# Optimization experiments

Hardware: AMD Instinct MI355X
Metric: run time of the kernel (lower is better)

## Reference

```python
import jax, jax.numpy as jnp
import numpy as np

EPS = 1e-08

def setup_inputs() -> dict:
    key = jax.random.key(0)
    k1, k2, k3, k4 = jax.random.split(key, 4)
    batch, n_in, n_out, D = 32768, 256, 512, 16
    x = jax.random.uniform(k1, (batch, n_in), jnp.float32, minval=-1.0, maxval=1.0)
    omega = jax.random.normal(k2, (D, 1), jnp.float32)          # stddev=1.0 init
    phase = 0.1 * jax.random.normal(k3, (D, 1), jnp.float32)    # zeros in module; small noise for non-degenerate test
    std_c = 1.0 / np.sqrt(n_in * D)
    c_basis = std_c * jax.random.normal(k4, (n_out, n_in, D), jnp.float32)
    bias = jnp.zeros((n_out,), jnp.float32)
    return {"x": x, "omega": omega, "phase": phase, "c_basis": c_basis, "bias": bias}

def _basis(x, omega, phase):
    # x: (batch, n_in) -> B: (batch, n_in, D)
    D = omega.shape[0]
    w = omega.reshape(1, 1, D)
    p = phase.reshape(1, 1, D)
    wx = w * x[..., None]
    s = jnp.sin(wx + p)
    mu = jnp.exp(-0.5 * w ** 2) * jnp.sin(p)
    std = jnp.sqrt(0.5 * (1.0 - jnp.exp(-2.0 * w ** 2) * jnp.cos(2.0 * p)) - mu ** 2)
    return (s + mu) / (std + EPS)

def reference(x, omega, phase, c_basis, bias):
    B = _basis(x, omega, phase)                     # (batch, n_in, D)
    y = jnp.einsum('bid,oid->bo', B, c_basis)       # (batch, n_out)
    return y + bias
```

## Files before the change

### kernel.cpp

```cpp
#include <hip/hip_runtime.h>
#include <hip/hip_bf16.h>


#define BATCH 32768
#define NIN   256
#define NOUT  512
#define DDIM  16
#define BM    128
#define BN    512
#define NKS   128
#define ASLICE 8192
#define BSLICE 32768
#define EPSV  1e-8f
#define INV2PI 0.15915494309189535f

typedef short  bf16x8 __attribute__((ext_vector_type(8)));
typedef float  f32x4  __attribute__((ext_vector_type(4)));

static __device__ __forceinline__ ushort f2bf(float f) {
  union { __hip_bfloat16 h; ushort u; } cv;
  cv.h = __float2bfloat16(f);
  return cv.u;
}

static __device__ __forceinline__ uint cvt_pk(float lo, float hi) {
  uint r;
  asm("v_cvt_pk_bf16_f32 %0, %1, %2" : "=v"(r) : "v"(lo), "v"(hi));
  return r;
}

__global__ __launch_bounds__(256) void prep_kernel(
    const float* __restrict__ omega, const float* __restrict__ phase,
    const float* __restrict__ c_basis, const float* __restrict__ bias,
    ushort* __restrict__ cb, float* __restrict__ offs)
{
  __shared__ float s_scale[DDIM];
  __shared__ float s_musc[DDIM];
  __shared__ float s_red[4];

  const int o = blockIdx.x;
  const int t = threadIdx.x;

  if (t < DDIM) {
    float w = omega[t];
    float p = phase[t];
    float mu  = expf(-0.5f * w * w) * sinf(p);
    float var = 0.5f * (1.0f - expf(-2.0f * w * w) * cosf(2.0f * p)) - mu * mu;
    float sd  = sqrtf(fmaxf(var, 0.0f));
    float sc  = 1.0f / (sd + EPSV);
    s_scale[t] = sc;
    s_musc[t]  = mu * sc;
  }
  __syncthreads();

  const float* cp = c_basis + ((size_t)o * NIN + t) * DDIM;
  float cv[DDIM];
  {
    const float4* cp4 = (const float4*)cp;
    float4 a = cp4[0], b = cp4[1], c = cp4[2], d = cp4[3];
    cv[0]=a.x; cv[1]=a.y; cv[2]=a.z; cv[3]=a.w;
    cv[4]=b.x; cv[5]=b.y; cv[6]=b.z; cv[7]=b.w;
    cv[8]=c.x; cv[9]=c.y; cv[10]=c.z; cv[11]=c.w;
    cv[12]=d.x; cv[13]=d.y; cv[14]=d.z; cv[15]=d.w;
  }

  float partial = 0.0f;
  uint pk[8];
#pragma unroll
  for (int d = 0; d < DDIM; d += 2) {
    partial += cv[d] * s_musc[d] + cv[d+1] * s_musc[d+1];
    ushort u0 = f2bf(cv[d]   * s_scale[d]);
    ushort u1 = f2bf(cv[d+1] * s_scale[d+1]);
    pk[d >> 1] = (uint)u0 | ((uint)u1 << 16);
  }

  {
    const int ks = t >> 1;
    const int h0 = (t & 1) * 2;
    const int fo = (o >> 1) & 3;
    char* rowp = (char*)cb + (size_t)ks * BSLICE + o * 64;
    *(uint4*)(rowp + ((h0    ) ^ fo) * 16) = make_uint4(pk[0], pk[1], pk[2], pk[3]);
    *(uint4*)(rowp + ((h0 + 1) ^ fo) * 16) = make_uint4(pk[4], pk[5], pk[6], pk[7]);
  }

#pragma unroll
  for (int off = 32; off > 0; off >>= 1) partial += __shfl_down(partial, off, 64);
  if ((t & 63) == 0) s_red[t >> 6] = partial;
  __syncthreads();
  if (t == 0) offs[o] = bias[o] + s_red[0] + s_red[1] + s_red[2] + s_red[3];
}

__global__ __launch_bounds__(512, 2) void gemm_kernel(
    const float* __restrict__ x, const float* __restrict__ omega,
    const float* __restrict__ phase, const ushort* __restrict__ cb,
    const float* __restrict__ offs, float* __restrict__ out)
{
  extern __shared__ char lds[];

  const int t    = threadIdx.x;
  const int lane = t & 63;
  const int wid  = t >> 6;
  const int wm   = wid >> 2;
  const int wn   = wid & 3;
  const int row0 = blockIdx.x * BM;

  f32x4 acc[4][8];
#pragma unroll
  for (int m = 0; m < 4; ++m)
#pragma unroll
    for (int n = 0; n < 8; ++n) acc[m][n] = (f32x4){0.f, 0.f, 0.f, 0.f};

  const int r   = t >> 2;
  const int sub = t & 3;
  const int il  = sub >> 1;
  const int d0  = (sub & 1) * 8;
  const float* xbase = x + (size_t)(row0 + r) * NIN + il;
  const int awa = r * 64 + ((sub ^ ((r >> 1) & 3)) * 16);

  float wvt[8], pvt[8];
#pragma unroll
  for (int j = 0; j < 8; ++j) {
    wvt[j] = omega[d0 + j] * INV2PI;
    pvt[j] = phase[d0 + j] * INV2PI;
  }

  const int hi  = lane >> 4;
  const int l15 = lane & 15;
  const int hu  = (hi ^ ((l15 >> 1) & 3)) * 16;

#define GLL(s_, d_) __builtin_amdgcn_global_load_lds(                          \
      (const __attribute__((address_space(1))) void*)(s_),                     \
      (__attribute__((address_space(3))) void*)(d_), 16, 0, 0)

#define ISSUE_B(ks_, slot_)                                                    \
  {                                                                            \
    const char* src = (const char*)cb + (size_t)(ks_) * BSLICE                 \
                      + wid * 1024 + lane * 16;                                \
    char* dst = lds + 32768 + (slot_) * BSLICE + wid * 1024;                   \
    GLL(src, dst);             GLL(src + 8192,  dst + 8192);                   \
    GLL(src + 16384, dst + 16384); GLL(src + 24576, dst + 24576);              \
  }

#define SINS4(xx_)                                                             \
    _Pragma("unroll")                                                          \
    for (int j = 0; j < 8; j += 2) {                                           \
      float s0 = __builtin_amdgcn_sinf(fmaf(wvt[j],     (xx_), pvt[j]));       \
      float s1 = __builtin_amdgcn_sinf(fmaf(wvt[j + 1], (xx_), pvt[j + 1]));   \
      pk[j >> 1] = cvt_pk(s0, s1);                                             \
    }

#define AWRITE(slot_)                                                          \
    *(uint4*)(lds + (slot_) * ASLICE + awa) = make_uint4(pk[0],pk[1],pk[2],pk[3]);

#define FRAG_MFMA(slot_)                                                       \
  {                                                                            \
    const char* AsB = lds + (slot_) * ASLICE;                                  \
    const char* BsB = lds + 32768 + (slot_) * BSLICE;                          \
    bf16x8 af[4];                                                              \
    _Pragma("unroll")                                                          \
    for (int m = 0; m < 4; ++m)                                                \
      af[m] = *(const bf16x8*)(AsB + (wm*64 + m*16 + l15) * 64 + hu);          \
    bf16x8 bfr[8];                                                             \
    _Pragma("unroll")                                                          \
    for (int n = 0; n < 8; ++n)                                                \
      bfr[n] = *(const bf16x8*)(BsB + (wn*128 + n*16 + l15) * 64 + hu);        \
    __builtin_amdgcn_s_setprio(1);                                             \
    _Pragma("unroll")                                                          \
    for (int m = 0; m < 4; ++m)                                                \
      _Pragma("unroll")                                                        \
      for (int n = 0; n < 8; ++n)                                              \
        acc[m][n] = __builtin_amdgcn_mfma_f32_16x16x32_bf16(af[m], bfr[n], acc[m][n], 0, 0, 0); \
    __builtin_amdgcn_s_setprio(0);                                             \
  }

#define BODY(s_, rd_, aw_, bg_, XU_, XL_)                                      \
  {                                                                            \
    ISSUE_B(((s_) + 3 < NKS ? (s_) + 3 : NKS - 1), bg_);                       \
    XL_ = xbase[((s_) + 3 < NKS ? (s_) + 3 : NKS - 1) * 2];                    \
    __builtin_amdgcn_sched_barrier(0);                                         \
    uint pk[4];                                                                \
    SINS4(XU_)                                                                 \
    AWRITE(aw_)                                                                \
    FRAG_MFMA(rd_)                                                             \
    __builtin_amdgcn_sched_barrier(0);                                         \
    asm volatile("s_waitcnt vmcnt(8) lgkmcnt(0)" ::: "memory");                \
    __builtin_amdgcn_s_barrier();                                              \
    __builtin_amdgcn_sched_barrier(0);                                         \
  }

  float xsA, xsB;
  {
    float xp0 = xbase[0];
    float xp1 = xbase[2];
    ISSUE_B(0, 0) ISSUE_B(1, 1) ISSUE_B(2, 2)
    xsA = xbase[4];
    uint pk[4];
    SINS4(xp0) AWRITE(0)
    SINS4(xp1) AWRITE(1)
    __builtin_amdgcn_sched_barrier(0);
    asm volatile("s_waitcnt vmcnt(0) lgkmcnt(0)" ::: "memory");
    __builtin_amdgcn_s_barrier();
    __builtin_amdgcn_sched_barrier(0);
  }

  for (int s = 0; s < NKS; s += 4) {
    BODY(s,     0, 2, 3, xsA, xsB)
    BODY(s + 1, 1, 3, 0, xsB, xsA)
    BODY(s + 2, 2, 0, 1, xsA, xsB)
    BODY(s + 3, 3, 1, 2, xsB, xsA)
  }

#pragma unroll
  for (int n = 0; n < 8; ++n) {
    int col = wn * 128 + n * 16 + l15;
    float off = offs[col];
#pragma unroll
    for (int m = 0; m < 4; ++m) {
      int row = row0 + wm * 64 + m * 16 + hi * 4;
      float* op = out + (size_t)row * NOUT + col;
#pragma unroll
      for (int j = 0; j < 4; ++j)
        op[(size_t)j * NOUT] = acc[m][n][j] + off;
    }
  }
}

extern "C" void kernel_launch(void* const* d_in, const int* in_sizes, int n_in,
                              void* d_out, int out_size, void* d_ws, size_t ws_size,
                              hipStream_t stream) {
  const float* x       = (const float*)d_in[0];
  const float* omega   = (const float*)d_in[1];
  const float* phase   = (const float*)d_in[2];
  const float* c_basis = (const float*)d_in[3];
  const float* bias    = (const float*)d_in[4];
  float* out = (float*)d_out;

  float*  offs = (float*)d_ws;
  ushort* cb   = (ushort*)((char*)d_ws + 2048);

  hipFuncSetAttribute((const void*)gemm_kernel,
                      hipFuncAttributeMaxDynamicSharedMemorySize, 163840);

  prep_kernel<<<NOUT, 256, 0, stream>>>(omega, phase, c_basis, bias, cb, offs);
  gemm_kernel<<<BATCH / BM, 512, 163840, stream>>>(x, omega, phase, cb, offs, out);
}
```

Baseline: 151.1 us.

## Compute A fragments in registers and give each wave private B slices without barriers

Each wave now computes its sin-basis A fragments straight into MFMA registers from x loads, instead of staging them through shared LDS. Each wave also double-buffers its own private slice of B, which removes all block-wide barriers. The block tile shrinks to 64 rows with 4 waves, and LDS use drops to 64KB. The cost is that every wave recomputes the same sines, four times redundant transcendental work per block, while B traffic per output row doubles because of the smaller BM and the prefetch depth drops from 3 to 1.

```diff
diff --git a/kernel.cpp b/kernel.cpp
--- a/kernel.cpp
+++ b/kernel.cpp
@@ -6,10 +6,9 @@
 #define NIN   256
 #define NOUT  512
 #define DDIM  16
-#define BM    128
+#define BM    64
 #define BN    512
 #define NKS   128
-#define ASLICE 8192
 #define BSLICE 32768
 #define EPSV  1e-8f
 #define INV2PI 0.15915494309189535f
@@ -90,7 +89,7 @@
   if (t == 0) offs[o] = bias[o] + s_red[0] + s_red[1] + s_red[2] + s_red[3];
 }
 
-__global__ __launch_bounds__(512, 2) void gemm_kernel(
+__global__ __launch_bounds__(256, 2) void gemm_kernel(
     const float* __restrict__ x, const float* __restrict__ omega,
     const float* __restrict__ phase, const ushort* __restrict__ cb,
     const float* __restrict__ offs, float* __restrict__ out)
@@ -99,35 +98,36 @@
 
   const int t    = threadIdx.x;
   const int lane = t & 63;
-  const int wid  = t >> 6;
-  const int wm   = wid >> 2;
-  const int wn   = wid & 3;
+  const int wn   = t >> 6;
   const int row0 = blockIdx.x * BM;
-
-  f32x4 acc[4][8];
-#pragma unroll
-  for (int m = 0; m < 4; ++m)
-#pragma unroll
-    for (int n = 0; n < 8; ++n) acc[m][n] = (f32x4){0.f, 0.f, 0.f, 0.f};
-
-  const int r   = t >> 2;
-  const int sub = t & 3;
-  const int il  = sub >> 1;
-  const int d0  = (sub & 1) * 8;
-  const float* xbase = x + (size_t)(row0 + r) * NIN + il;
-  const int awa = r * 64 + ((sub ^ ((r >> 1) & 3)) * 16);
-
-  float wvt[8], pvt[8];
-#pragma unroll
-  for (int j = 0; j < 8; ++j) {
-    wvt[j] = omega[d0 + j] * INV2PI;
-    pvt[j] = phase[d0 + j] * INV2PI;
-  }
 
   const int hi  = lane >> 4;
   const int l15 = lane & 15;
   const int hu  = (hi ^ ((l15 >> 1) & 3)) * 16;
 
+  float wl[8], pl[8];
+  {
+    const int dbase = (hi & 1) * 8;
+#pragma unroll
+    for (int j = 0; j < 8; ++j) {
+      wl[j] = omega[dbase + j] * INV2PI;
+      pl[j] = phase[dbase + j] * INV2PI;
+    }
+  }
+
+  const float* xp0 = x + (size_t)(row0 + 0 * 16 + l15) * NIN;
+  const float* xp1 = x + (size_t)(row0 + 1 * 16 + l15) * NIN;
+  const float* xp2 = x + (size_t)(row0 + 2 * 16 + l15) * NIN;
+  const float* xp3 = x + (size_t)(row0 + 3 * 16 + l15) * NIN;
+
+  f32x4 acc[4][8];
+#pragma unroll
+  for (int m = 0; m < 4; ++m)
+#pragma unroll
+    for (int n = 0; n < 8; ++n) acc[m][n] = (f32x4){0.f, 0.f, 0.f, 0.f};
+
+  char* ldsW = lds + wn * 16384;
+
 #define GLL(s_, d_) __builtin_amdgcn_global_load_lds(                          \
       (const __attribute__((address_space(1))) void*)(s_),                     \
       (__attribute__((address_space(3))) void*)(d_), 16, 0, 0)
@@ -135,35 +135,50 @@
 #define ISSUE_B(ks_, slot_)                                                    \
   {                                                                            \
     const char* src = (const char*)cb + (size_t)(ks_) * BSLICE                 \
-                      + wid * 1024 + lane * 16;                                \
-    char* dst = lds + 32768 + (slot_) * BSLICE + wid * 1024;                   \
-    GLL(src, dst);             GLL(src + 8192,  dst + 8192);                   \
-    GLL(src + 16384, dst + 16384); GLL(src + 24576, dst + 24576);              \
-  }
-
-#define SINS4(xx_)                                                             \
-    _Pragma("unroll")                                                          \
-    for (int j = 0; j < 8; j += 2) {                                           \
-      float s0 = __builtin_amdgcn_sinf(fmaf(wvt[j],     (xx_), pvt[j]));       \
-      float s1 = __builtin_amdgcn_sinf(fmaf(wvt[j + 1], (xx_), pvt[j + 1]));   \
-      pk[j >> 1] = cvt_pk(s0, s1);                                             \
-    }
-
-#define AWRITE(slot_)                                                          \
-    *(uint4*)(lds + (slot_) * ASLICE + awa) = make_uint4(pk[0],pk[1],pk[2],pk[3]);
-
-#define FRAG_MFMA(slot_)                                                       \
+                      + wn * 8192 + lane * 16;                                 \
+    char* dst = ldsW + (slot_) * 8192;                                         \
+    GLL(src, dst);               GLL(src + 1024, dst + 1024);                  \
+    GLL(src + 2048, dst + 2048); GLL(src + 3072, dst + 3072);                  \
+    GLL(src + 4096, dst + 4096); GLL(src + 5120, dst + 5120);                  \
+    GLL(src + 6144, dst + 6144); GLL(src + 7168, dst + 7168);                  \
+  }
+
+#define XLOAD(XV_, s_)                                                         \
+    XV_[0] = *(const float2*)(xp0 + 2 * (s_));                                 \
+    XV_[1] = *(const float2*)(xp1 + 2 * (s_));                                 \
+    XV_[2] = *(const float2*)(xp2 + 2 * (s_));                                 \
+    XV_[3] = *(const float2*)(xp3 + 2 * (s_));
+
+#define MAKE_AF(m_, XV_)                                                       \
   {                                                                            \
-    const char* AsB = lds + (slot_) * ASLICE;                                  \
-    const char* BsB = lds + 32768 + (slot_) * BSLICE;                          \
+    float xx = (hi & 2) ? XV_[m_].y : XV_[m_].x;                               \
+    uint w0 = cvt_pk(__builtin_amdgcn_sinf(fmaf(wl[0], xx, pl[0])),            \
+                     __builtin_amdgcn_sinf(fmaf(wl[1], xx, pl[1])));           \
+    uint w1 = cvt_pk(__builtin_amdgcn_sinf(fmaf(wl[2], xx, pl[2])),            \
+                     __builtin_amdgcn_sinf(fmaf(wl[3], xx, pl[3])));           \
+    uint w2 = cvt_pk(__builtin_amdgcn_sinf(fmaf(wl[4], xx, pl[4])),            \
+                     __builtin_amdgcn_sinf(fmaf(wl[5], xx, pl[5])));           \
+    uint w3 = cvt_pk(__builtin_amdgcn_sinf(fmaf(wl[6], xx, pl[6])),            \
+                     __builtin_amdgcn_sinf(fmaf(wl[7], xx, pl[7])));           \
+    uint2 lohi0 = make_uint2(w0, w1), lohi1 = make_uint2(w2, w3);              \
+    af[m_] = __builtin_bit_cast(bf16x8,                                        \
+              make_uint4(lohi0.x, lohi0.y, lohi1.x, lohi1.y));                 \
+  }
+
+#define BODY(s_, sl_, XU_, XL_)                                                \
+  {                                                                            \
+    const int ksn = ((s_) + 1 < NKS ? (s_) + 1 : NKS - 1);                     \
+    ISSUE_B(ksn, (sl_) ^ 1)                                                    \
+    XLOAD(XL_, ksn)                                                            \
+    __builtin_amdgcn_sched_barrier(0);                                         \
+    asm volatile("s_waitcnt vmcnt(16)" ::: "memory");                          \
     bf16x8 af[4];                                                              \
-    _Pragma("unroll")                                                          \
-    for (int m = 0; m < 4; ++m)                                                \
-      af[m] = *(const bf16x8*)(AsB + (wm*64 + m*16 + l15) * 64 + hu);          \
+    MAKE_AF(0, XU_) MAKE_AF(1, XU_) MAKE_AF(2, XU_) MAKE_AF(3, XU_)            \
+    const char* BsB = ldsW + (sl_) * 8192;                                     \
     bf16x8 bfr[8];                                                             \
     _Pragma("unroll")                                                          \
     for (int n = 0; n < 8; ++n)                                                \
-      bfr[n] = *(const bf16x8*)(BsB + (wn*128 + n*16 + l15) * 64 + hu);        \
+      bfr[n] = *(const bf16x8*)(BsB + (n * 16 + l15) * 64 + hu);               \
     __builtin_amdgcn_s_setprio(1);                                             \
     _Pragma("unroll")                                                          \
     for (int m = 0; m < 4; ++m)                                                \
@@ -173,41 +188,14 @@
     __builtin_amdgcn_s_setprio(0);                                             \
   }
 
-#define BODY(s_, rd_, aw_, bg_, XU_, XL_)                                      \
-  {                                                                            \
-    ISSUE_B(((s_) + 3 < NKS ? (s_) + 3 : NKS - 1), bg_);                       \
-    XL_ = xbase[((s_) + 3 < NKS ? (s_) + 3 : NKS - 1) * 2];                    \
-    __builtin_amdgcn_sched_barrier(0);                                         \
-    uint pk[4];                                                                \
-    SINS4(XU_)                                                                 \
-    AWRITE(aw_)                                                                \
-    FRAG_MFMA(rd_)                                                             \
-    __builtin_amdgcn_sched_barrier(0);                                         \
-    asm volatile("s_waitcnt vmcnt(8) lgkmcnt(0)" ::: "memory");                \
-    __builtin_amdgcn_s_barrier();                                              \
-    __builtin_amdgcn_sched_barrier(0);                                         \
-  }
-
-  float xsA, xsB;
-  {
-    float xp0 = xbase[0];
-    float xp1 = xbase[2];
-    ISSUE_B(0, 0) ISSUE_B(1, 1) ISSUE_B(2, 2)
-    xsA = xbase[4];
-    uint pk[4];
-    SINS4(xp0) AWRITE(0)
-    SINS4(xp1) AWRITE(1)
-    __builtin_amdgcn_sched_barrier(0);
-    asm volatile("s_waitcnt vmcnt(0) lgkmcnt(0)" ::: "memory");
-    __builtin_amdgcn_s_barrier();
-    __builtin_amdgcn_sched_barrier(0);
-  }
-
-  for (int s = 0; s < NKS; s += 4) {
-    BODY(s,     0, 2, 3, xsA, xsB)
-    BODY(s + 1, 1, 3, 0, xsB, xsA)
-    BODY(s + 2, 2, 0, 1, xsA, xsB)
-    BODY(s + 3, 3, 1, 2, xsB, xsA)
+  float2 xvA[4], xvB[4];
+
+  ISSUE_B(0, 0)
+  XLOAD(xvA, 0)
+
+  for (int s = 0; s < NKS; s += 2) {
+    BODY(s,     0, xvA, xvB)
+    BODY(s + 1, 1, xvB, xvA)
   }
 
 #pragma unroll
@@ -216,7 +204,7 @@
     float off = offs[col];
 #pragma unroll
     for (int m = 0; m < 4; ++m) {
-      int row = row0 + wm * 64 + m * 16 + hi * 4;
+      int row = row0 + m * 16 + hi * 4;
       float* op = out + (size_t)row * NOUT + col;
 #pragma unroll
       for (int j = 0; j < 4; ++j)
@@ -239,8 +227,8 @@
   ushort* cb   = (ushort*)((char*)d_ws + 2048);
 
   hipFuncSetAttribute((const void*)gemm_kernel,
-                      hipFuncAttributeMaxDynamicSharedMemorySize, 163840);
+                      hipFuncAttributeMaxDynamicSharedMemorySize, 65536);
 
   prep_kernel<<<NOUT, 256, 0, stream>>>(omega, phase, c_basis, bias, cb, offs);
-  gemm_kernel<<<BATCH / BM, 512, 163840, stream>>>(x, omega, phase, cb, offs, out);
-}
+  gemm_kernel<<<BATCH / BM, 256, 65536, stream>>>(x, omega, phase, cb, offs, out);
+}
```

New measurement: 194.5 us. 1.29x slower.
